# Kernel optimization log

Measured on AMD Instinct MI355X. Metric: run time of the kernel, lower is better.

Reference implementation:

```python
import jax, jax.numpy as jnp
import numpy as np

N_HEADS = 16
HEAD_DIM = 64
D_MODEL = N_HEADS * HEAD_DIM
MASK_NUM = -2.0**32 + 1.0
LN_EPS = 1e-8


def setup_inputs() -> dict:
    key = jax.random.key(0)
    ks = jax.random.split(key, 6)
    B, S = 2, 2048
    queries = jax.random.normal(ks[0], (B, S, D_MODEL), dtype=jnp.float32)
    keys = jax.random.normal(ks[1], (B, S, D_MODEL), dtype=jnp.float32)
    values = jax.random.normal(ks[2], (B, S, D_MODEL), dtype=jnp.float32)
    lim = np.sqrt(6.0 / (D_MODEL + D_MODEL)).astype(np.float32)  # glorot_uniform
    Wq = jax.random.uniform(ks[3], (D_MODEL, D_MODEL), jnp.float32, -lim, lim)
    Wk = jax.random.uniform(ks[4], (D_MODEL, D_MODEL), jnp.float32, -lim, lim)
    Wv = jax.random.uniform(ks[5], (D_MODEL, D_MODEL), jnp.float32, -lim, lim)
    gamma = jnp.ones((D_MODEL,), jnp.float32)
    beta = jnp.zeros((D_MODEL,), jnp.float32)
    return {"queries": queries, "keys": keys, "values": values,
            "Wq": Wq, "Wk": Wk, "Wv": Wv, "gamma": gamma, "beta": beta}


def _split_heads(x):
    # [B, S, H*dh] -> tf.split(axis=2)+concat(axis=0) order: [H*B, S, dh]
    B, S, _ = x.shape
    return x.reshape(B, S, N_HEADS, HEAD_DIM).transpose(2, 0, 1, 3).reshape(N_HEADS * B, S, HEAD_DIM)


def _merge_heads(x, B):
    # [H*B, S, dh] -> [B, S, H*dh]
    S = x.shape[1]
    return x.reshape(N_HEADS, B, S, HEAD_DIM).transpose(1, 2, 0, 3).reshape(B, S, D_MODEL)


def reference(queries, keys, values, Wq, Wk, Wv, gamma, beta):
    B = queries.shape[0]
    q = _split_heads(queries @ Wq)   # [HB, Sq, dh]
    k = _split_heads(keys @ Wk)      # [HB, Sk, dh]
    v = _split_heads(values @ Wv)    # [HB, Sk, dh]

    scores = jnp.einsum('bqd,bkd->bqk', q, k) / jnp.float32(np.sqrt(HEAD_DIM))
    # key padding mask: positions whose projected key is all-zero
    kmask = jnp.sign(jnp.sum(jnp.abs(k), axis=-1))  # [HB, Sk]
    scores = jnp.where(kmask[:, None, :] == 0, jnp.float32(MASK_NUM), scores)
    attn = jax.nn.softmax(scores, axis=-1)
    # query mask: zero out rows whose projected query is all-zero
    qmask = jnp.sign(jnp.sum(jnp.abs(q), axis=-1))  # [HB, Sq]
    attn = attn * qmask[:, :, None]
    att_out = jnp.einsum('bqk,bkd->bqd', attn, v)   # [HB, Sq, dh]
    att_out = _merge_heads(att_out, B)               # [B, Sq, D]

    x = att_out + queries
    mean = jnp.mean(x, axis=-1, keepdims=True)
    var = jnp.mean((x - mean) ** 2, axis=-1, keepdims=True)
    norm = (x - mean) / jnp.sqrt(var + LN_EPS)
    return gamma * norm + beta
```

## Files before the change

### kernel.cpp

```cpp
#include <hip/hip_runtime.h>

#define DM   1024
#define SEQ  2048
#define NH   16
#define HD   64
#define ROWS 4096

typedef unsigned short u16;
typedef unsigned int   u32;
typedef __attribute__((ext_vector_type(8))) __bf16 bf16x8;
typedef __attribute__((ext_vector_type(4))) float  f32x4;
typedef __attribute__((ext_vector_type(16))) float f32x16;

__device__ __forceinline__ u16 f2bf(float f) {
  u32 u = __builtin_bit_cast(u32, f);
  u += 0x7fffu + ((u >> 16) & 1u);
  return (u16)(u >> 16);
}

__device__ __forceinline__ void async16(const void* g, void* lds) {
  __builtin_amdgcn_global_load_lds((const __attribute__((address_space(1))) u32*)g,
                                   (__attribute__((address_space(3))) u32*)lds, 16, 0, 0);
}


__global__ __launch_bounds__(256) void k_cvt_act(const float* __restrict__ q,
                                                 const float* __restrict__ k,
                                                 const float* __restrict__ v,
                                                 u16* __restrict__ dst) {
  const float* src = blockIdx.z == 0 ? q : (blockIdx.z == 1 ? k : v);
  u16* d = dst + (size_t)blockIdx.z * ((size_t)ROWS * DM);
  size_t i = ((size_t)blockIdx.x * 256 + threadIdx.x) * 8;
  float4 a = *(const float4*)(src + i);
  float4 b = *(const float4*)(src + i + 4);
  u32 w0 = (u32)f2bf(a.x) | ((u32)f2bf(a.y) << 16);
  u32 w1 = (u32)f2bf(a.z) | ((u32)f2bf(a.w) << 16);
  u32 w2 = (u32)f2bf(b.x) | ((u32)f2bf(b.y) << 16);
  u32 w3 = (u32)f2bf(b.z) | ((u32)f2bf(b.w) << 16);
  uint4 o4; o4.x = w0; o4.y = w1; o4.z = w2; o4.w = w3;
  *(uint4*)(d + i) = o4;
}

__global__ __launch_bounds__(256) void k_cvt_wt(const float* __restrict__ Wq,
                                                const float* __restrict__ Wk,
                                                const float* __restrict__ Wv,
                                                u16* __restrict__ wt) {
  __shared__ float t[32][33];
  const float* W = blockIdx.z == 0 ? Wq : (blockIdx.z == 1 ? Wk : Wv);
  u16* D = wt + (size_t)blockIdx.z * (DM * DM);
  int bx = blockIdx.x * 32, by = blockIdx.y * 32;
  int x = threadIdx.x, y = threadIdx.y;
  for (int i = 0; i < 32; i += 8) t[y + i][x] = W[(size_t)(by + y + i) * DM + bx + x];
  __syncthreads();
  for (int i = 0; i < 32; i += 8) D[(size_t)(bx + y + i) * DM + by + x] = f2bf(t[x][y + i]);
}


__global__ __launch_bounds__(512) void k_gemm(const u16* __restrict__ Abase,
                                              const u16* __restrict__ Btbase,
                                              u16* __restrict__ Cbase) {
  __shared__ u16 As[2][256 * 64];
  __shared__ u16 Bs[2][256 * 64];
  const int z = blockIdx.z;
  const u16* A  = Abase  + (size_t)z * ((size_t)ROWS * DM);
  const u16* Bt = Btbase + (size_t)z * (DM * DM);
  u16* C        = Cbase  + (size_t)z * ((size_t)ROWS * DM);
  const float sc = (z == 0) ? 0.18033688011112043f : 1.0f;
  const int tid = threadIdx.x, w = tid >> 6, l = tid & 63;
  const int fr = l & 15, fq = l >> 4;
  int bid = blockIdx.y * 4 + blockIdx.x;
  int nb  = (bid & 7) * 8 + (bid >> 3);
  int m0 = (nb >> 2) * 256, n0 = (nb & 3) * 256;
  int wr = (w >> 2) * 128, wc = (w & 3) * 64;
  f32x4 acc[8][4];
  for (int i = 0; i < 8; ++i) for (int j = 0; j < 4; ++j) acc[i][j] = (f32x4){0.f, 0.f, 0.f, 0.f};

  u32 aoff[4], boff[4];
#pragma unroll
  for (int i = 0; i < 4; ++i) {
    int c = i * 512 + tid;
    int row = c >> 3, blk = c & 7;
    int gblk = blk ^ (row & 7);
    aoff[i] = (u32)((m0 + row) * DM + gblk * 8);
    boff[i] = (u32)((n0 + row) * DM + gblk * 8);
  }

#pragma unroll
  for (int i = 0; i < 4; ++i) {
    async16(A  + aoff[i], (char*)As[0] + (i * 512 + tid) * 16);
    async16(Bt + boff[i], (char*)Bs[0] + (i * 512 + tid) * 16);
  }

  for (int t = 0; t < 16; ++t) {
    const int cur = t & 1, nxt = cur ^ 1;
    {
      u32 kk = (t + 1 < 16) ? (u32)(t + 1) * 64u : 15u * 64u;
#pragma unroll
      for (int i = 0; i < 4; ++i) {
        async16(A  + kk + aoff[i], (char*)As[nxt] + (i * 512 + tid) * 16);
        async16(Bt + kk + boff[i], (char*)Bs[nxt] + (i * 512 + tid) * 16);
      }
    }
    asm volatile("s_waitcnt vmcnt(8)" ::: "memory");
    __builtin_amdgcn_s_barrier();
    asm volatile("" ::: "memory");

#pragma unroll
    for (int ks = 0; ks < 2; ++ks) {
      bf16x8 af[8], bf[4];
#pragma unroll
      for (int i = 0; i < 8; ++i) {
        int row = wr + i * 16 + fr;
        af[i] = *(const bf16x8*)(&As[cur][row * 64 + (((ks * 4 + fq) ^ (row & 7)) << 3)]);
      }
#pragma unroll
      for (int j = 0; j < 4; ++j) {
        int row = wc + j * 16 + fr;
        bf[j] = *(const bf16x8*)(&Bs[cur][row * 64 + (((ks * 4 + fq) ^ (row & 7)) << 3)]);
      }
      __builtin_amdgcn_s_setprio(1);
#pragma unroll
      for (int i = 0; i < 8; ++i)
#pragma unroll
        for (int j = 0; j < 4; ++j)
          acc[i][j] = __builtin_amdgcn_mfma_f32_16x16x32_bf16(af[i], bf[j], acc[i][j], 0, 0, 0);
      __builtin_amdgcn_s_setprio(0);
    }

    asm volatile("" ::: "memory");
    __builtin_amdgcn_s_barrier();
    asm volatile("" ::: "memory");
  }

  for (int i = 0; i < 8; ++i)
    for (int j = 0; j < 4; ++j)
      for (int jj = 0; jj < 4; ++jj) {
        int row = m0 + wr + i * 16 + fq * 4 + jj;
        int col = n0 + wc + j * 16 + fr;
        C[(size_t)row * DM + col] = f2bf(acc[i][j][jj] * sc);
      }
}


__global__ __launch_bounds__(256) void k_vt(const u16* __restrict__ vproj,
                                            u16* __restrict__ vt) {
  __shared__ u16 t[64][64];
  int y = blockIdx.y;
  int h = y >> 1, b = y & 1;
  int s0 = blockIdx.x * 64;
  int tid = threadIdx.x;
  for (int c = 0; c < 2; ++c) {
    int rr = c * 32 + (tid >> 3);
    int blk = tid & 7;
    uint4 vv = *(const uint4*)(vproj + (size_t)(b * SEQ + s0 + rr) * DM + h * 64 + blk * 8);
    *(uint4*)(&t[rr][((blk ^ (rr & 7)) * 8)]) = vv;
  }
  __syncthreads();
  for (int c = 0; c < 2; ++c) {
    int d = c * 32 + (tid >> 3);
    int p = tid & 7;
    int B = p ^ (d & 7);
    int g = B >> 1, half = B & 1;
    u16 tmp[8];
    for (int j = 0; j < 8; ++j) {
      int kj = (j < 4) ? (4 * half + j) : (8 + 4 * half + (j - 4));
      int ss = 16 * g + kj;
      tmp[j] = t[ss][((d >> 3) ^ (ss & 7)) * 8 + (d & 7)];
    }
    *(uint4*)(vt + (size_t)(y * 64 + d) * SEQ + s0 + p * 8) = *(uint4*)tmp;
  }
}


__global__ __launch_bounds__(256, 2) void k_attn(const u16* __restrict__ Qp,
                                                 const u16* __restrict__ Kp,
                                                 const u16* __restrict__ Vt,
                                                 u16* __restrict__ attb) {
  __shared__ u16 lds[20480];
  const int tid = threadIdx.x, w = tid >> 6, l = tid & 63;
  const int lrow = l & 31, h = l >> 5;
  const int kh = w & 1, qg = w >> 1;
  const int g = blockIdx.x;
  const int vy = (g & 7) * 4 + ((g >> 3) & 3);
  const int vx = g >> 5;
  const int head = vy >> 1, b = vy & 1;
  const int hcol = head * 64;
  const int q0w = vx * 128 + qg * 64;

  bf16x8 qb00, qb01, qb02, qb03, qb10, qb11, qb12, qb13;
  {
    const u16* qr0 = Qp + (size_t)(b * SEQ + q0w + lrow) * DM + hcol + h * 8;
    qb00 = *(const bf16x8*)(qr0);
    qb01 = *(const bf16x8*)(qr0 + 16);
    qb02 = *(const bf16x8*)(qr0 + 32);
    qb03 = *(const bf16x8*)(qr0 + 48);
    const u16* qr1 = Qp + (size_t)(b * SEQ + q0w + 32 + lrow) * DM + hcol + h * 8;
    qb10 = *(const bf16x8*)(qr1);
    qb11 = *(const bf16x8*)(qr1 + 16);
    qb12 = *(const bf16x8*)(qr1 + 32);
    qb13 = *(const bf16x8*)(qr1 + 48);
  }

  const int sw = lrow & 7;
  const int kbase = kh * 4096 + lrow * 128;
  const int B0 = kbase + (((0 + h) ^ sw) << 4);
  const int B1 = kbase + (((2 + h) ^ sw) << 4);
  const int B2 = kbase + (((4 + h) ^ sw) << 4);
  const int B3 = kbase + (((6 + h) ^ sw) << 4);

  const int vfb = lrow * 128;
  const int V0 = vfb + (((4 * kh + 0 + h) ^ sw) << 4);
  const int V1 = vfb + (((4 * kh + 2 + h) ^ sw) << 4);

  const int ldo0 = w * 1024, ldo1 = (4 + w) * 1024;
  const int e0 = (ldo0 >> 1) + l * 8, e1 = (ldo1 >> 1) + l * 8;
  const int r0 = e0 >> 6, r1 = e1 >> 6;
  const int kb0 = ((e0 & 63) >> 3) ^ (r0 & 7), kb1 = ((e1 & 63) >> 3) ^ (r1 & 7);
  const u32 koff0 = (u32)((b * SEQ + r0) * DM + hcol + kb0 * 8);
  const u32 koff1 = (u32)((b * SEQ + r1) * DM + hcol + kb1 * 8);
  const u32 voff0 = (u32)((vy * 64 + r0) * SEQ + (e0 & 63));
  const u32 voff1 = (u32)((vy * 64 + r1) * SEQ + (e1 & 63));

  const f32x16 kzero = {};
  f32x16 ot00 = {}, ot01 = {}, ot10 = {}, ot11 = {};
  float lacc0 = 0.f, lacc1 = 0.f;
  bf16x8 pb00 = {}, pb01 = {}, pb10 = {}, pb11 = {};

  char* base = (char*)lds;
  async16(Kp + koff0, base + ldo0);
  async16(Kp + koff1, base + ldo1);
  async16(Vt + voff0, base + 16384 + ldo0);
  async16(Vt + voff1, base + 16384 + ldo1);

  int vwr = 1, vcr = 0, vrd = 2;
  for (int t = 0; t < SEQ / 64; ++t) {
    {
      u32 u = (t + 1 < SEQ / 64) ? (u32)(t + 1) : (u32)(SEQ / 64 - 1);
      u32 kadv = u * (64 * DM);
      u32 vadv = u * 64;
      char* kd = base + ((t + 1) & 1) * 8192;
      char* vd = base + 16384 + vwr * 8192;
      async16(Kp + kadv + koff0, kd + ldo0);
      async16(Kp + kadv + koff1, kd + ldo1);
      async16(Vt + vadv + voff0, vd + ldo0);
      async16(Vt + vadv + voff1, vd + ldo1);
    }
    asm volatile("s_waitcnt vmcnt(6)" ::: "memory");
    __builtin_amdgcn_s_barrier();
    asm volatile("" ::: "memory");

    const char* Kb = base + (t & 1) * 8192;
    bf16x8 a0 = *(const bf16x8*)(Kb + B0);
    bf16x8 a1 = *(const bf16x8*)(Kb + B1);
    bf16x8 a2 = *(const bf16x8*)(Kb + B2);
    bf16x8 a3 = *(const bf16x8*)(Kb + B3);
    __builtin_amdgcn_s_setprio(1);
    f32x16 st0 = __builtin_amdgcn_mfma_f32_32x32x16_bf16(a0, qb00, kzero, 0, 0, 0);
    f32x16 st1 = __builtin_amdgcn_mfma_f32_32x32x16_bf16(a0, qb10, kzero, 0, 0, 0);
    st0 = __builtin_amdgcn_mfma_f32_32x32x16_bf16(a1, qb01, st0, 0, 0, 0);
    st1 = __builtin_amdgcn_mfma_f32_32x32x16_bf16(a1, qb11, st1, 0, 0, 0);
    st0 = __builtin_amdgcn_mfma_f32_32x32x16_bf16(a2, qb02, st0, 0, 0, 0);
    st1 = __builtin_amdgcn_mfma_f32_32x32x16_bf16(a2, qb12, st1, 0, 0, 0);
    st0 = __builtin_amdgcn_mfma_f32_32x32x16_bf16(a3, qb03, st0, 0, 0, 0);
    st1 = __builtin_amdgcn_mfma_f32_32x32x16_bf16(a3, qb13, st1, 0, 0, 0);
    __builtin_amdgcn_s_setprio(0);

    if (t) {
      const char* Vb = base + 16384 + vrd * 8192;
      bf16x8 vf0 = *(const bf16x8*)(Vb + V0);
      bf16x8 vf1 = *(const bf16x8*)(Vb + V1);
      bf16x8 vf2 = *(const bf16x8*)(Vb + 4096 + V0);
      bf16x8 vf3 = *(const bf16x8*)(Vb + 4096 + V1);
      __builtin_amdgcn_s_setprio(1);
      ot00 = __builtin_amdgcn_mfma_f32_32x32x16_bf16(vf0, pb00, ot00, 0, 0, 0);
      ot10 = __builtin_amdgcn_mfma_f32_32x32x16_bf16(vf0, pb10, ot10, 0, 0, 0);
      ot00 = __builtin_amdgcn_mfma_f32_32x32x16_bf16(vf1, pb01, ot00, 0, 0, 0);
      ot10 = __builtin_amdgcn_mfma_f32_32x32x16_bf16(vf1, pb11, ot10, 0, 0, 0);
      ot01 = __builtin_amdgcn_mfma_f32_32x32x16_bf16(vf2, pb00, ot01, 0, 0, 0);
      ot11 = __builtin_amdgcn_mfma_f32_32x32x16_bf16(vf2, pb10, ot11, 0, 0, 0);
      ot01 = __builtin_amdgcn_mfma_f32_32x32x16_bf16(vf3, pb01, ot01, 0, 0, 0);
      ot11 = __builtin_amdgcn_mfma_f32_32x32x16_bf16(vf3, pb11, ot11, 0, 0, 0);
      __builtin_amdgcn_s_setprio(0);
    }

    {
      f32x16 p;
#pragma unroll
      for (int i = 0; i < 16; ++i) p[i] = __builtin_amdgcn_exp2f(st0[i]);
      float s0 = (p[0] + p[1]) + (p[2] + p[3]);
      float s1 = (p[4] + p[5]) + (p[6] + p[7]);
      float s2 = (p[8] + p[9]) + (p[10] + p[11]);
      float s3 = (p[12] + p[13]) + (p[14] + p[15]);
      lacc0 += (s0 + s1) + (s2 + s3);
#pragma unroll
      for (int j = 0; j < 8; ++j) { pb00[j] = (__bf16)p[j]; pb01[j] = (__bf16)p[8 + j]; }
    }
    {
      f32x16 p;
#pragma unroll
      for (int i = 0; i < 16; ++i) p[i] = __builtin_amdgcn_exp2f(st1[i]);
      float s0 = (p[0] + p[1]) + (p[2] + p[3]);
      float s1 = (p[4] + p[5]) + (p[6] + p[7]);
      float s2 = (p[8] + p[9]) + (p[10] + p[11]);
      float s3 = (p[12] + p[13]) + (p[14] + p[15]);
      lacc1 += (s0 + s1) + (s2 + s3);
#pragma unroll
      for (int j = 0; j < 8; ++j) { pb10[j] = (__bf16)p[j]; pb11[j] = (__bf16)p[8 + j]; }
    }

    asm volatile("" ::: "memory");
    __builtin_amdgcn_s_barrier();
    asm volatile("" ::: "memory");

    int tmp = vrd; vrd = vcr; vcr = vwr; vwr = tmp;
  }

  asm volatile("s_waitcnt vmcnt(0)" ::: "memory");
  __builtin_amdgcn_s_barrier();
  asm volatile("" ::: "memory");
  {
    const char* Vb = base + 16384 + vrd * 8192;
    bf16x8 vf0 = *(const bf16x8*)(Vb + V0);
    bf16x8 vf1 = *(const bf16x8*)(Vb + V1);
    bf16x8 vf2 = *(const bf16x8*)(Vb + 4096 + V0);
    bf16x8 vf3 = *(const bf16x8*)(Vb + 4096 + V1);
    ot00 = __builtin_amdgcn_mfma_f32_32x32x16_bf16(vf0, pb00, ot00, 0, 0, 0);
    ot10 = __builtin_amdgcn_mfma_f32_32x32x16_bf16(vf0, pb10, ot10, 0, 0, 0);
    ot00 = __builtin_amdgcn_mfma_f32_32x32x16_bf16(vf1, pb01, ot00, 0, 0, 0);
    ot10 = __builtin_amdgcn_mfma_f32_32x32x16_bf16(vf1, pb11, ot10, 0, 0, 0);
    ot01 = __builtin_amdgcn_mfma_f32_32x32x16_bf16(vf2, pb00, ot01, 0, 0, 0);
    ot11 = __builtin_amdgcn_mfma_f32_32x32x16_bf16(vf2, pb10, ot11, 0, 0, 0);
    ot01 = __builtin_amdgcn_mfma_f32_32x32x16_bf16(vf3, pb01, ot01, 0, 0, 0);
    ot11 = __builtin_amdgcn_mfma_f32_32x32x16_bf16(vf3, pb11, ot11, 0, 0, 0);
  }
  lacc0 += __shfl_xor(lacc0, 32);
  lacc1 += __shfl_xor(lacc1, 32);

  __syncthreads();
  float* mrg = (float*)lds;
  const int slot = qg * 4352;
  if (kh) {
#pragma unroll
    for (int r = 0; r < 16; ++r) {
      mrg[slot + r * 64 + l] = ot00[r];
      mrg[slot + (16 + r) * 64 + l] = ot01[r];
      mrg[slot + (32 + r) * 64 + l] = ot10[r];
      mrg[slot + (48 + r) * 64 + l] = ot11[r];
    }
    mrg[slot + 4096 + l] = lacc0;
    mrg[slot + 4160 + l] = lacc1;
  }
  __syncthreads();
  if (!kh) {
    float inv0 = 1.f / (lacc0 + mrg[slot + 4096 + l]);
    float inv1 = 1.f / (lacc1 + mrg[slot + 4160 + l]);
    u16* orow0 = attb + (size_t)(b * SEQ + q0w + lrow) * DM + hcol + 4 * h;
    u16* orow1 = attb + (size_t)(b * SEQ + q0w + 32 + lrow) * DM + hcol + 4 * h;
#pragma unroll
    for (int G = 0; G < 4; ++G) {
      uint2 o;
      o.x = (u32)f2bf((ot00[4*G+0] + mrg[slot + (4*G+0)*64 + l]) * inv0)
          | ((u32)f2bf((ot00[4*G+1] + mrg[slot + (4*G+1)*64 + l]) * inv0) << 16);
      o.y = (u32)f2bf((ot00[4*G+2] + mrg[slot + (4*G+2)*64 + l]) * inv0)
          | ((u32)f2bf((ot00[4*G+3] + mrg[slot + (4*G+3)*64 + l]) * inv0) << 16);
      *(uint2*)(orow0 + 8 * G) = o;
      uint2 o1;
      o1.x = (u32)f2bf((ot01[4*G+0] + mrg[slot + (16+4*G+0)*64 + l]) * inv0)
           | ((u32)f2bf((ot01[4*G+1] + mrg[slot + (16+4*G+1)*64 + l]) * inv0) << 16);
      o1.y = (u32)f2bf((ot01[4*G+2] + mrg[slot + (16+4*G+2)*64 + l]) * inv0)
           | ((u32)f2bf((ot01[4*G+3] + mrg[slot + (16+4*G+3)*64 + l]) * inv0) << 16);
      *(uint2*)(orow0 + 32 + 8 * G) = o1;
      uint2 o2;
      o2.x = (u32)f2bf((ot10[4*G+0] + mrg[slot + (32+4*G+0)*64 + l]) * inv1)
           | ((u32)f2bf((ot10[4*G+1] + mrg[slot + (32+4*G+1)*64 + l]) * inv1) << 16);
      o2.y = (u32)f2bf((ot10[4*G+2] + mrg[slot + (32+4*G+2)*64 + l]) * inv1)
           | ((u32)f2bf((ot10[4*G+3] + mrg[slot + (32+4*G+3)*64 + l]) * inv1) << 16);
      *(uint2*)(orow1 + 8 * G) = o2;
      uint2 o3;
      o3.x = (u32)f2bf((ot11[4*G+0] + mrg[slot + (48+4*G+0)*64 + l]) * inv1)
           | ((u32)f2bf((ot11[4*G+1] + mrg[slot + (48+4*G+1)*64 + l]) * inv1) << 16);
      o3.y = (u32)f2bf((ot11[4*G+2] + mrg[slot + (48+4*G+2)*64 + l]) * inv1)
           | ((u32)f2bf((ot11[4*G+3] + mrg[slot + (48+4*G+3)*64 + l]) * inv1) << 16);
      *(uint2*)(orow1 + 32 + 8 * G) = o3;
    }
  }
}


__global__ __launch_bounds__(256) void k_ln(const u16* __restrict__ attb,
                                            const float* __restrict__ qin,
                                            const float* __restrict__ gamma,
                                            const float* __restrict__ beta,
                                            float* __restrict__ out) {
  __shared__ float rsum[4], rsum2[4];
  int row = blockIdx.x, t = threadIdx.x;
  size_t off = (size_t)row * DM + t * 4;
  uint2 av = *(const uint2*)(attb + off);
  float4 a;
  a.x = __builtin_bit_cast(float, av.x << 16);
  a.y = __builtin_bit_cast(float, av.x & 0xffff0000u);
  a.z = __builtin_bit_cast(float, av.y << 16);
  a.w = __builtin_bit_cast(float, av.y & 0xffff0000u);
  float4 q = *(const float4*)(qin + off);
  float4 x; x.x = a.x + q.x; x.y = a.y + q.y; x.z = a.z + q.z; x.w = a.w + q.w;
  float s = x.x + x.y + x.z + x.w;
  float s2 = x.x * x.x + x.y * x.y + x.z * x.z + x.w * x.w;
  for (int o2 = 1; o2 < 64; o2 <<= 1) { s += __shfl_xor(s, o2); s2 += __shfl_xor(s2, o2); }
  int w = t >> 6, l = t & 63;
  if (l == 0) { rsum[w] = s; rsum2[w] = s2; }
  __syncthreads();
  s = rsum[0] + rsum[1] + rsum[2] + rsum[3];
  s2 = rsum2[0] + rsum2[1] + rsum2[2] + rsum2[3];
  float mean = s * (1.f / DM);
  float var = s2 * (1.f / DM) - mean * mean;
  float rstd = rsqrtf(var + 1e-8f);
  float4 g = *(const float4*)(gamma + t * 4);
  float4 be = *(const float4*)(beta + t * 4);
  float4 r;
  r.x = (x.x - mean) * rstd * g.x + be.x;
  r.y = (x.y - mean) * rstd * g.y + be.y;
  r.z = (x.z - mean) * rstd * g.z + be.z;
  r.w = (x.w - mean) * rstd * g.w + be.w;
  *(float4*)(out + off) = r;
}


extern "C" void kernel_launch(void* const* d_in, const int* in_sizes, int n_in,
                              void* d_out, int out_size, void* d_ws, size_t ws_size,
                              hipStream_t stream) {
  (void)in_sizes; (void)n_in; (void)out_size; (void)ws_size;
  const float* q     = (const float*)d_in[0];
  const float* k     = (const float*)d_in[1];
  const float* v     = (const float*)d_in[2];
  const float* Wq    = (const float*)d_in[3];
  const float* Wk    = (const float*)d_in[4];
  const float* Wv    = (const float*)d_in[5];
  const float* gamma = (const float*)d_in[6];
  const float* beta  = (const float*)d_in[7];
  float* out = (float*)d_out;
  char* ws = (char*)d_ws;

  const size_t ACT_B = 3ull * ROWS * DM * 2;
  const size_t WT_B  = 3ull * DM * DM * 2;

  u16* actb  = (u16*)ws;
  u16* wtb   = (u16*)(ws + ACT_B);
  u16* projb = (u16*)(ws + ACT_B + WT_B);
  u16* vt    = (u16*)ws;
  u16* attb  = (u16*)(ws + 8ull * 1024 * 1024);

  k_cvt_act<<<dim3(2048, 1, 3), 256, 0, stream>>>(q, k, v, actb);
  k_cvt_wt<<<dim3(32, 32, 3), dim3(32, 8), 0, stream>>>(Wq, Wk, Wv, wtb);
  k_gemm<<<dim3(4, 16, 3), 512, 0, stream>>>(actb, wtb, projb);
  k_vt<<<dim3(SEQ / 64, NH * 2), 256, 0, stream>>>(projb + 2ull * ROWS * DM, vt);
  k_attn<<<512, 256, 0, stream>>>(projb, projb + (size_t)ROWS * DM, vt, attb);
  k_ln<<<ROWS, 256, 0, stream>>>(attb, q, gamma, beta, out);
}
```

Baseline: 110.5 us.

## Fuse fp32-to-bf16 activation conversion into projection GEMM A-tile loads

Removes the separate activation conversion kernel and has the projection GEMM read fp32 activations directly, converting them to bf16 in registers and storing them swizzled into LDS. The A loads are register-prefetched one k-tile ahead while B keeps async global-to-LDS loads. This cuts a full bf16 write and re-read of three 4096x1024 activation tensors and one launch. The cost is twice the global bytes per A tile inside the GEMM, more registers, and conversion ALU work in the main loop, which may reduce latency hiding. The workspace layout is rearranged so the V-transpose and attention buffers no longer alias the removed activation buffer.

```diff
diff --git a/kernel.cpp b/kernel.cpp
--- a/kernel.cpp
+++ b/kernel.cpp
@@ -21,24 +21,6 @@
 __device__ __forceinline__ void async16(const void* g, void* lds) {
   __builtin_amdgcn_global_load_lds((const __attribute__((address_space(1))) u32*)g,
                                    (__attribute__((address_space(3))) u32*)lds, 16, 0, 0);
-}
-
-
-__global__ __launch_bounds__(256) void k_cvt_act(const float* __restrict__ q,
-                                                 const float* __restrict__ k,
-                                                 const float* __restrict__ v,
-                                                 u16* __restrict__ dst) {
-  const float* src = blockIdx.z == 0 ? q : (blockIdx.z == 1 ? k : v);
-  u16* d = dst + (size_t)blockIdx.z * ((size_t)ROWS * DM);
-  size_t i = ((size_t)blockIdx.x * 256 + threadIdx.x) * 8;
-  float4 a = *(const float4*)(src + i);
-  float4 b = *(const float4*)(src + i + 4);
-  u32 w0 = (u32)f2bf(a.x) | ((u32)f2bf(a.y) << 16);
-  u32 w1 = (u32)f2bf(a.z) | ((u32)f2bf(a.w) << 16);
-  u32 w2 = (u32)f2bf(b.x) | ((u32)f2bf(b.y) << 16);
-  u32 w3 = (u32)f2bf(b.z) | ((u32)f2bf(b.w) << 16);
-  uint4 o4; o4.x = w0; o4.y = w1; o4.z = w2; o4.w = w3;
-  *(uint4*)(d + i) = o4;
 }
 
 __global__ __launch_bounds__(256) void k_cvt_wt(const float* __restrict__ Wq,
@@ -56,13 +38,15 @@
 }
 
 
-__global__ __launch_bounds__(512) void k_gemm(const u16* __restrict__ Abase,
+__global__ __launch_bounds__(512) void k_gemm(const float* __restrict__ qf,
+                                              const float* __restrict__ kf,
+                                              const float* __restrict__ vf,
                                               const u16* __restrict__ Btbase,
                                               u16* __restrict__ Cbase) {
   __shared__ u16 As[2][256 * 64];
   __shared__ u16 Bs[2][256 * 64];
   const int z = blockIdx.z;
-  const u16* A  = Abase  + (size_t)z * ((size_t)ROWS * DM);
+  const float* A = z == 0 ? qf : (z == 1 ? kf : vf);
   const u16* Bt = Btbase + (size_t)z * (DM * DM);
   u16* C        = Cbase  + (size_t)z * ((size_t)ROWS * DM);
   const float sc = (z == 0) ? 0.18033688011112043f : 1.0f;
@@ -75,33 +59,78 @@
   f32x4 acc[8][4];
   for (int i = 0; i < 8; ++i) for (int j = 0; j < 4; ++j) acc[i][j] = (f32x4){0.f, 0.f, 0.f, 0.f};
 
-  u32 aoff[4], boff[4];
+  const int r0 = tid >> 3, ablk = tid & 7;
+  const int aswz = ((ablk ^ (r0 & 7)) << 3);
+  size_t aidx[4];
+  int    awr_[4];
+  u32    boff[4];
 #pragma unroll
   for (int i = 0; i < 4; ++i) {
-    int c = i * 512 + tid;
-    int row = c >> 3, blk = c & 7;
-    int gblk = blk ^ (row & 7);
-    aoff[i] = (u32)((m0 + row) * DM + gblk * 8);
+    int row = i * 64 + r0;
+    aidx[i] = (size_t)(m0 + row) * DM + ablk * 8;
+    awr_[i] = row * 64 + aswz;
+    int gblk = ablk ^ (row & 7);
     boff[i] = (u32)((n0 + row) * DM + gblk * 8);
   }
 
+  float4 pl[4], ph[4];
+
 #pragma unroll
   for (int i = 0; i < 4; ++i) {
-    async16(A  + aoff[i], (char*)As[0] + (i * 512 + tid) * 16);
+    pl[i] = *(const float4*)(A + aidx[i]);
+    ph[i] = *(const float4*)(A + aidx[i] + 4);
+  }
+#pragma unroll
+  for (int i = 0; i < 4; ++i) {
+    uint4 o;
+    o.x = (u32)f2bf(pl[i].x) | ((u32)f2bf(pl[i].y) << 16);
+    o.y = (u32)f2bf(pl[i].z) | ((u32)f2bf(pl[i].w) << 16);
+    o.z = (u32)f2bf(ph[i].x) | ((u32)f2bf(ph[i].y) << 16);
+    o.w = (u32)f2bf(ph[i].z) | ((u32)f2bf(ph[i].w) << 16);
+    *(uint4*)(&As[0][awr_[i]]) = o;
+  }
+#pragma unroll
+  for (int i = 0; i < 4; ++i)
     async16(Bt + boff[i], (char*)Bs[0] + (i * 512 + tid) * 16);
-  }
+#pragma unroll
+  for (int i = 0; i < 4; ++i) {
+    pl[i] = *(const float4*)(A + aidx[i] + 64);
+    ph[i] = *(const float4*)(A + aidx[i] + 68);
+  }
+  asm volatile("s_waitcnt vmcnt(0) lgkmcnt(0)" ::: "memory");
+  __builtin_amdgcn_s_barrier();
 
   for (int t = 0; t < 16; ++t) {
     const int cur = t & 1, nxt = cur ^ 1;
     {
       u32 kk = (t + 1 < 16) ? (u32)(t + 1) * 64u : 15u * 64u;
 #pragma unroll
+      for (int i = 0; i < 4; ++i)
+        async16(Bt + kk + boff[i], (char*)Bs[nxt] + (i * 512 + tid) * 16);
+    }
+    if (t + 1 < 16) {
+#pragma unroll
       for (int i = 0; i < 4; ++i) {
-        async16(A  + kk + aoff[i], (char*)As[nxt] + (i * 512 + tid) * 16);
-        async16(Bt + kk + boff[i], (char*)Bs[nxt] + (i * 512 + tid) * 16);
+        uint4 o;
+        o.x = (u32)f2bf(pl[i].x) | ((u32)f2bf(pl[i].y) << 16);
+        o.y = (u32)f2bf(pl[i].z) | ((u32)f2bf(pl[i].w) << 16);
+        o.z = (u32)f2bf(ph[i].x) | ((u32)f2bf(ph[i].y) << 16);
+        o.w = (u32)f2bf(ph[i].z) | ((u32)f2bf(ph[i].w) << 16);
+        *(uint4*)(&As[nxt][awr_[i]]) = o;
       }
-    }
-    asm volatile("s_waitcnt vmcnt(8)" ::: "memory");
+      if (t + 2 < 16) {
+        u32 kk2 = (u32)(t + 2) * 64u;
+#pragma unroll
+        for (int i = 0; i < 4; ++i) {
+          pl[i] = *(const float4*)(A + aidx[i] + kk2);
+          ph[i] = *(const float4*)(A + aidx[i] + kk2 + 4);
+        }
+      }
+    } else {
+      asm volatile("s_waitcnt vmcnt(0)" ::: "memory");
+    }
+
+    asm volatile("s_waitcnt lgkmcnt(0)" ::: "memory");
     __builtin_amdgcn_s_barrier();
     asm volatile("" ::: "memory");
 
@@ -440,18 +469,17 @@
   float* out = (float*)d_out;
   char* ws = (char*)d_ws;
 
-  const size_t ACT_B = 3ull * ROWS * DM * 2;
-  const size_t WT_B  = 3ull * DM * DM * 2;
-
-  u16* actb  = (u16*)ws;
-  u16* wtb   = (u16*)(ws + ACT_B);
-  u16* projb = (u16*)(ws + ACT_B + WT_B);
-  u16* vt    = (u16*)ws;
-  u16* attb  = (u16*)(ws + 8ull * 1024 * 1024);
-
-  k_cvt_act<<<dim3(2048, 1, 3), 256, 0, stream>>>(q, k, v, actb);
+  const size_t WT_B   = 3ull * DM * DM * 2;
+  const size_t PROJ_B = 3ull * ROWS * DM * 2;
+  const size_t VT_B   = (size_t)NH * 2 * HD * SEQ * 2;
+
+  u16* wtb   = (u16*)ws;
+  u16* projb = (u16*)(ws + WT_B);
+  u16* vt    = (u16*)(ws + WT_B + PROJ_B);
+  u16* attb  = (u16*)(ws + WT_B + PROJ_B + VT_B);
+
   k_cvt_wt<<<dim3(32, 32, 3), dim3(32, 8), 0, stream>>>(Wq, Wk, Wv, wtb);
-  k_gemm<<<dim3(4, 16, 3), 512, 0, stream>>>(actb, wtb, projb);
+  k_gemm<<<dim3(4, 16, 3), 512, 0, stream>>>(q, k, v, wtb, projb);
   k_vt<<<dim3(SEQ / 64, NH * 2), 256, 0, stream>>>(projb + 2ull * ROWS * DM, vt);
   k_attn<<<512, 256, 0, stream>>>(projb, projb + (size_t)ROWS * DM, vt, attb);
   k_ln<<<ROWS, 256, 0, stream>>>(attb, q, gamma, beta, out);
```

After: 106.6 us. 1.04x faster.
